# Optimization experiments

Hardware: AMD Instinct MI355X
Metric: run time of the kernel (lower is better)

## Reference

```python
import jax, jax.numpy as jnp
import numpy as np

N_NODES = 100000
N_EDGES = 3200000
F_IN = 128
F_HID = 32
F_OUT = 40


def gcn_conv(x, edge_index, edge_weight, W, b):
    # GCNConv with normalize=False: linear transform, then edge-weighted
    # gather from source nodes and scatter-add into destination nodes.
    h = x @ W                                   # [N, F_out]
    src, dst = edge_index[0], edge_index[1]
    msgs = h[src] * edge_weight[:, None]        # [E, F_out] gather + scale
    agg = jax.ops.segment_sum(msgs, dst, num_segments=N_NODES)
    return agg + b


def setup_inputs() -> dict:
    key = jax.random.key(0)
    k1, k2, k3, k4, k5, k6, k7 = jax.random.split(key, 7)
    x = jax.random.normal(k1, (N_NODES, F_IN), dtype=jnp.float32)
    edge_index = jax.random.randint(k2, (2, N_EDGES), 0, N_NODES, dtype=jnp.int64)
    edge_weight = jax.random.uniform(k3, (N_EDGES,), dtype=jnp.float32)
    # Glorot-style init for layer weights, zeros for biases (PyG defaults)
    W1 = jax.random.normal(k4, (F_IN, F_HID), dtype=jnp.float32) * (1.0 / np.sqrt(F_IN))
    b1 = jnp.zeros((F_HID,), dtype=jnp.float32)
    W2 = jax.random.normal(k5, (F_HID, F_OUT), dtype=jnp.float32) * (1.0 / np.sqrt(F_HID))
    b2 = jnp.zeros((F_OUT,), dtype=jnp.float32)
    return {"x": x, "edge_index": edge_index, "edge_weight": edge_weight,
            "W1": W1, "b1": b1, "W2": W2, "b2": b2}


def reference(x, edge_index, edge_weight, W1, b1, W2, b2):
    h = gcn_conv(x, edge_index, edge_weight, W1, b1)
    h = jax.nn.relu(h)
    # F.dropout(training=self.training) is identity in eval mode
    h = gcn_conv(h, edge_index, edge_weight, W2, b2)
    return jax.nn.log_softmax(h, axis=1)
```

## Files before the change

### kernel.cpp

```cpp
#include <hip/hip_runtime.h>
#include <hip/hip_fp16.h>
#include <math.h>

#define N_NODES 100000
#define N_EDGES 3200000
#define F_IN    128
#define F_HID   32
#define F_OUT   40
#define NBINS   ((N_NODES + 255) >> 8)
#define EPB     4096
#define NBLK    ((N_EDGES + EPB - 1) / EPB)
#define BKT_CAP (N_EDGES + 8 * N_NODES)

typedef _Float16 h2_t __attribute__((ext_vector_type(2)));
__device__ __forceinline__ float fdot2u(unsigned a, unsigned b, float c) {
    return __builtin_amdgcn_fdot2(__builtin_bit_cast(h2_t, a),
                                  __builtin_bit_cast(h2_t, b), c, false);
}

__global__ __launch_bounds__(256) void gemm1_kernel(const float* __restrict__ x,
                                                    const float* __restrict__ W,
                                                    __half* __restrict__ h1h) {
    __shared__ float Ws[F_IN * F_HID];
    __shared__ float Xs[32][F_IN + 4];
    const int tid  = threadIdx.x;
    const int row0 = blockIdx.x * 32;

    for (int i = tid; i < (F_IN * F_HID) / 4; i += 256)
        ((float4*)Ws)[i] = ((const float4*)W)[i];

    for (int i = tid; i < 1024; i += 256) {
        int r = i >> 5;
        int c = i & 31;
        ((float4*)&Xs[r][0])[c] = ((const float4*)x)[(size_t)(row0 + r) * (F_IN / 4) + c];
    }
    __syncthreads();

    const int r  = tid >> 3;
    const int c0 = (tid & 7) * 4;
    float a0 = 0.f, a1 = 0.f, a2 = 0.f, a3 = 0.f;
    for (int k = 0; k < F_IN; ++k) {
        const float xv = Xs[r][k];
        const float* wrow = &Ws[k * F_HID + c0];
        a0 += xv * wrow[0];
        a1 += xv * wrow[1];
        a2 += xv * wrow[2];
        a3 += xv * wrow[3];
    }
    const int row = row0 + r;
    __half2* o = (__half2*)(h1h + (size_t)row * F_HID + c0);
    o[0] = __floats2half2_rn(a0, a1);
    o[1] = __floats2half2_rn(a2, a3);
}

__global__ __launch_bounds__(256) void histA_kernel(const int* __restrict__ ei,
                                                    int* __restrict__ gcnt) {
    __shared__ int lh[NBINS];
    const int tid = threadIdx.x;
    const int e0  = blockIdx.x * EPB;
    for (int i = tid; i < NBINS; i += 256) lh[i] = 0;
    __syncthreads();

    for (int base = 0; base < EPB; base += 1024) {
        const int e = e0 + base + 4 * tid;
        if (e + 3 < N_EDGES) {
            const int4 dv = *(const int4*)&ei[N_EDGES + e];
            atomicAdd(&lh[dv.x >> 8], 1);
            atomicAdd(&lh[dv.y >> 8], 1);
            atomicAdd(&lh[dv.z >> 8], 1);
            atomicAdd(&lh[dv.w >> 8], 1);
        } else {
            for (int k = 0; k < 4; ++k)
                if (e + k < N_EDGES) atomicAdd(&lh[ei[N_EDGES + e + k] >> 8], 1);
        }
    }
    __syncthreads();
    for (int b = tid; b < NBINS; b += 256)
        gcnt[(size_t)blockIdx.x * NBINS + b] = lh[b];
}

__global__ __launch_bounds__(256) void colscan_kernel(const int* __restrict__ gcnt,
                                                      int* __restrict__ pbase,
                                                      int* __restrict__ bintot) {
    __shared__ int s[256];
    __shared__ int carry;
    const int b   = blockIdx.x;
    const int tid = threadIdx.x;
    if (tid == 0) carry = 0;
    __syncthreads();
    for (int c = 0; c < NBLK; c += 256) {
        const int blk = c + tid;
        const int v = (blk < NBLK) ? gcnt[(size_t)blk * NBINS + b] : 0;
        s[tid] = v;
        __syncthreads();
        for (int off = 1; off < 256; off <<= 1) {
            int u = (tid >= off) ? s[tid - off] : 0;
            __syncthreads();
            s[tid] += u;
            __syncthreads();
        }
        if (blk < NBLK) pbase[(size_t)blk * NBINS + b] = carry + s[tid] - v;
        __syncthreads();
        if (tid == 255) carry += s[255];
        __syncthreads();
    }
    if (tid == 0) bintot[b] = carry;
}

__global__ __launch_bounds__(512) void binscan_kernel(const int* __restrict__ bintot,
                                                      int* __restrict__ binbase) {
    __shared__ int s[512];
    const int t = threadIdx.x;
    const int v = (t < NBINS) ? bintot[t] : 0;
    s[t] = v;
    __syncthreads();
    for (int off = 1; off < 512; off <<= 1) {
        int u = (t >= off) ? s[t - off] : 0;
        __syncthreads();
        s[t] += u;
        __syncthreads();
    }
    if (t <= NBINS) binbase[t] = s[t] - v;
}

__global__ __launch_bounds__(256) void placeA_kernel(const int* __restrict__ ei,
                                                     const float* __restrict__ ew,
                                                     const int* __restrict__ gcnt,
                                                     const int* __restrict__ binbase,
                                                     const int* __restrict__ pbase,
                                                     int* __restrict__ stg4,
                                                     unsigned char* __restrict__ dlowg) {
    __shared__ int lhist[512];
    __shared__ int lscan[512];
    __shared__ int lcur[512];
    __shared__ int lwbase[512];
    __shared__ int stmp[256];
    __shared__ int lstg4[EPB];
    __shared__ unsigned short lbin[EPB];
    __shared__ unsigned char ldlow[EPB];
    const int tid = threadIdx.x;
    const int blk = blockIdx.x;
    const int e0  = blk * EPB;
    const int tot = min(EPB, N_EDGES - e0);

    lhist[tid] = 0; lhist[tid + 256] = 0;
    lwbase[tid] = 0; lwbase[tid + 256] = 0;
    __syncthreads();
    for (int b = tid; b < NBINS; b += 256) {
        lhist[b]  = gcnt[(size_t)blk * NBINS + b];
        lwbase[b] = binbase[b] + pbase[(size_t)blk * NBINS + b];
    }
    __syncthreads();

    const int ca = lhist[2 * tid];
    const int cb = lhist[2 * tid + 1];
    const int pair = ca + cb;
    stmp[tid] = pair;
    __syncthreads();
    for (int off = 1; off < 256; off <<= 1) {
        int u = (tid >= off) ? stmp[tid - off] : 0;
        __syncthreads();
        stmp[tid] += u;
        __syncthreads();
    }
    const int pexcl = stmp[tid] - pair;
    lscan[2 * tid]     = pexcl;
    lscan[2 * tid + 1] = pexcl + ca;
    lcur[2 * tid]      = pexcl;
    lcur[2 * tid + 1]  = pexcl + ca;
    __syncthreads();

#define PLACE1(S, D, WF)                                                        \
    {                                                                           \
        const int b = (D) >> 8;                                                 \
        const int p = atomicAdd(&lcur[b], 1);                                   \
        lstg4[p] = (S) | ((int)__half_as_ushort(__float2half(WF)) << 17);       \
        lbin[p] = (unsigned short)b;                                            \
        ldlow[p] = (unsigned char)((D) & 255);                                  \
    }
    for (int base = 0; base < EPB; base += 1024) {
        const int e = e0 + base + 4 * tid;
        if (e + 3 < N_EDGES) {
            const int4   sv = *(const int4*)&ei[e];
            const int4   dv = *(const int4*)&ei[N_EDGES + e];
            const float4 wv = *(const float4*)&ew[e];
            PLACE1(sv.x, dv.x, wv.x);
            PLACE1(sv.y, dv.y, wv.y);
            PLACE1(sv.z, dv.z, wv.z);
            PLACE1(sv.w, dv.w, wv.w);
        } else {
            for (int k = 0; k < 4; ++k)
                if (e + k < N_EDGES)
                    PLACE1(ei[e + k], ei[N_EDGES + e + k], ew[e + k]);
        }
    }
#undef PLACE1
    __syncthreads();

    for (int i = tid; i < tot; i += 256) {
        const int b = lbin[i];
        const int pos = lwbase[b] + (i - lscan[b]);
        stg4[pos] = lstg4[i];
        dlowg[pos] = ldlow[i];
    }
}

__global__ __launch_bounds__(256) void partB1_kernel(const int* __restrict__ binbase,
                                                     const unsigned char* __restrict__ dlowg,
                                                     int* __restrict__ offsIB,
                                                     int* __restrict__ pbt) {
    __shared__ int lcnt[256];
    __shared__ int lsc[256];
    const int tid   = threadIdx.x;
    const int b     = blockIdx.x;
    const int start = binbase[b];
    const int end   = binbase[b + 1];

    lcnt[tid] = 0;
    __syncthreads();
    for (int j = start + tid; j < end; j += 256)
        atomicAdd(&lcnt[dlowg[j]], 1);
    __syncthreads();

    const int padded = (lcnt[tid] + 7) & ~7;
    lsc[tid] = padded;
    __syncthreads();
    for (int off = 1; off < 256; off <<= 1) {
        int u = (tid >= off) ? lsc[tid - off] : 0;
        __syncthreads();
        lsc[tid] += u;
        __syncthreads();
    }
    offsIB[(b << 8) + tid] = lsc[tid] - padded;
    if (tid == 255) pbt[b] = lsc[255];
}

__global__ __launch_bounds__(512) void padscan_kernel(const int* __restrict__ pbt,
                                                      int* __restrict__ pbb,
                                                      int* __restrict__ offs) {
    __shared__ int s[512];
    const int t = threadIdx.x;
    const int v = (t < NBINS) ? pbt[t] : 0;
    s[t] = v;
    __syncthreads();
    for (int off = 1; off < 512; off <<= 1) {
        int u = (t >= off) ? s[t - off] : 0;
        __syncthreads();
        s[t] += u;
        __syncthreads();
    }
    const int excl = s[t] - v;
    if (t <= NBINS) pbb[t] = excl;
    if (t == NBINS) offs[N_NODES] = excl;
}

__global__ __launch_bounds__(256) void partB2_kernel(const int* __restrict__ binbase,
                                                     const int* __restrict__ stg4,
                                                     const unsigned char* __restrict__ dlowg,
                                                     const int* __restrict__ pbb,
                                                     const int* __restrict__ offsIB,
                                                     int* __restrict__ offs,
                                                     int* __restrict__ bkt) {
    __shared__ int lcur[256];
    const int tid  = threadIdx.x;
    const int b    = blockIdx.x;
    const int node = (b << 8) + tid;
    const int base = pbb[b] + offsIB[node];
    const int pend = (tid < 255) ? (pbb[b] + offsIB[node + 1]) : pbb[b + 1];
    lcur[tid] = base;
    if (node < N_NODES) offs[node] = base;
    __syncthreads();

    const int start = binbase[b];
    const int end   = binbase[b + 1];
    for (int j = start + tid; j < end; j += 256) {
        const int word = stg4[j];
        const int pos = atomicAdd(&lcur[dlowg[j]], 1);
        bkt[pos] = word;
    }
    __syncthreads();

    for (int k = lcur[tid]; k < pend; ++k) bkt[k] = 0;
}

__device__ __forceinline__ void gather_grp(const int* __restrict__ bkt,
                                           int j, const int jend,
                                           const char* __restrict__ tbl,
                                           const unsigned sub8,
                                           float& a0, float& a1, float& a2, float& a3) {
#define PAIR_BODY(PX, PY, RA, RB)                                               \
    {                                                                           \
        const unsigned wp = __builtin_amdgcn_perm((unsigned)(PY) >> 17,         \
                                                  (unsigned)(PX) >> 17,         \
                                                  0x05040100u);                 \
        a0 = fdot2u(__builtin_amdgcn_perm((RB).x, (RA).x, 0x05040100u), wp, a0);\
        a1 = fdot2u(__builtin_amdgcn_perm((RB).x, (RA).x, 0x07060302u), wp, a1);\
        a2 = fdot2u(__builtin_amdgcn_perm((RB).y, (RA).y, 0x05040100u), wp, a2);\
        a3 = fdot2u(__builtin_amdgcn_perm((RB).y, (RA).y, 0x07060302u), wp, a3);\
    }
#define TBL(P) (*(const uint2*)(tbl + (((unsigned)(P) & 0x1FFFFu) << 6) + sub8))
    for (; j < jend; j += 8) {
        const int4 p0 = *(const int4*)&bkt[j];
        const int4 p1 = *(const int4*)&bkt[j + 4];
        const uint2 r0 = TBL(p0.x);
        const uint2 r1 = TBL(p0.y);
        const uint2 r2 = TBL(p0.z);
        const uint2 r3 = TBL(p0.w);
        const uint2 r4 = TBL(p1.x);
        const uint2 r5 = TBL(p1.y);
        const uint2 r6 = TBL(p1.z);
        const uint2 r7 = TBL(p1.w);
        PAIR_BODY(p0.x, p0.y, r0, r1);
        PAIR_BODY(p0.z, p0.w, r2, r3);
        PAIR_BODY(p1.x, p1.y, r4, r5);
        PAIR_BODY(p1.z, p1.w, r6, r7);
    }
#undef TBL
#undef PAIR_BODY
}

__global__ __launch_bounds__(256) void gather1_kernel(const int* __restrict__ offs,
                                                      const int* __restrict__ bkt,
                                                      const __half* __restrict__ h1h,
                                                      const float* __restrict__ b1,
                                                      __half* __restrict__ rh) {
    const int tid  = threadIdx.x;
    const int node = blockIdx.x * 32 + (tid >> 3);
    const int sub  = tid & 7;
    const unsigned sub8 = sub * 8;

    float a0 = 0.f, a1 = 0.f, a2 = 0.f, a3 = 0.f;
    gather_grp(bkt, offs[node], offs[node + 1], (const char*)h1h, sub8,
               a0, a1, a2, a3);

    const float4 bb = ((const float4*)b1)[sub];
    a0 = fmaxf(a0 + bb.x, 0.f);
    a1 = fmaxf(a1 + bb.y, 0.f);
    a2 = fmaxf(a2 + bb.z, 0.f);
    a3 = fmaxf(a3 + bb.w, 0.f);
    uint2 o;
    *(__half2*)&o.x = __floats2half2_rn(a0, a1);
    *(__half2*)&o.y = __floats2half2_rn(a2, a3);
    *(uint2*)((char*)rh + (size_t)node * 64 + sub8) = o;
}

__global__ __launch_bounds__(256) void gather2_lsm_kernel(const int* __restrict__ offs,
                                                          const int* __restrict__ bkt,
                                                          const __half* __restrict__ rh,
                                                          const float* __restrict__ W2,
                                                          const float* __restrict__ b2,
                                                          float* __restrict__ out) {
    __shared__ float W2s[F_HID * F_OUT];
    __shared__ float sblk[32][F_HID + 1];
    const int tid = threadIdx.x;
    for (int i = tid; i < F_HID * F_OUT; i += 256) W2s[i] = W2[i];
    __syncthreads();

    const int nn   = tid >> 3;
    const int node = blockIdx.x * 32 + nn;
    const int sub  = tid & 7;
    const unsigned sub8 = sub * 8;

    float a0 = 0.f, a1 = 0.f, a2 = 0.f, a3 = 0.f;
    gather_grp(bkt, offs[node], offs[node + 1], (const char*)rh, sub8,
               a0, a1, a2, a3);

    sblk[nn][sub * 4 + 0] = a0;
    sblk[nn][sub * 4 + 1] = a1;
    sblk[nn][sub * 4 + 2] = a2;
    sblk[nn][sub * 4 + 3] = a3;

    float o0 = b2[sub], o1 = b2[sub + 8], o2 = b2[sub + 16],
          o3 = b2[sub + 24], o4 = b2[sub + 32];
    #pragma unroll
    for (int k = 0; k < F_HID; ++k) {
        const float sv = sblk[nn][k];
        const float* wr = &W2s[k * F_OUT + sub];
        o0 += sv * wr[0];
        o1 += sv * wr[8];
        o2 += sv * wr[16];
        o3 += sv * wr[24];
        o4 += sv * wr[32];
    }

    float m = fmaxf(fmaxf(fmaxf(o0, o1), fmaxf(o2, o3)), o4);
    m = fmaxf(m, __shfl_xor(m, 1));
    m = fmaxf(m, __shfl_xor(m, 2));
    m = fmaxf(m, __shfl_xor(m, 4));
    float ex = __expf(o0 - m) + __expf(o1 - m) + __expf(o2 - m)
             + __expf(o3 - m) + __expf(o4 - m);
    ex += __shfl_xor(ex, 1);
    ex += __shfl_xor(ex, 2);
    ex += __shfl_xor(ex, 4);
    const float ls = m + __logf(ex);

    float* op = out + (size_t)node * F_OUT + sub;
    op[0]  = o0 - ls;
    op[8]  = o1 - ls;
    op[16] = o2 - ls;
    op[24] = o3 - ls;
    op[32] = o4 - ls;
}

extern "C" void kernel_launch(void* const* d_in, const int* in_sizes, int n_in,
                              void* d_out, int out_size, void* d_ws, size_t ws_size,
                              hipStream_t stream) {
    const float* x  = (const float*)d_in[0];
    const int*   ei = (const int*)d_in[1];
    const float* ew = (const float*)d_in[2];
    const float* W1 = (const float*)d_in[3];
    const float* b1 = (const float*)d_in[4];
    const float* W2 = (const float*)d_in[5];
    const float* b2 = (const float*)d_in[6];
    float* out = (float*)d_out;

    char* p = (char*)d_ws;
    size_t off = 0;
    auto alloc = [&](size_t bytes) {
        char* r = p + off;
        off += (bytes + 15) & ~(size_t)15;
        return r;
    };
    int*   gcnt    = (int*)  alloc((size_t)NBLK * NBINS * 4);
    int*   pbase   = (int*)  alloc((size_t)NBLK * NBINS * 4);
    int*   bintot  = (int*)  alloc((size_t)NBINS * 4);
    int*   binbase = (int*)  alloc((size_t)(NBINS + 1) * 4);
    int*   pbt     = (int*)  alloc((size_t)NBINS * 4);
    int*   pbb     = (int*)  alloc((size_t)(NBINS + 1) * 4);
    int*   offsIB  = (int*)  alloc((size_t)NBINS * 256 * 4);
    int*   offs    = (int*)  alloc((size_t)(N_NODES + 1) * 4);
    int*   bkt     = (int*)  alloc((size_t)BKT_CAP * 4);
    char*  uni     = (char*) alloc((size_t)N_EDGES * 5);
    int*   stg4    = (int*)uni;
    unsigned char* dlowg = (unsigned char*)(uni + (size_t)N_EDGES * 4);
    __half* h1h    = (__half*)uni;
    __half* rh     = h1h + (size_t)N_NODES * F_HID;

    histA_kernel<<<NBLK, 256, 0, stream>>>(ei, gcnt);
    colscan_kernel<<<NBINS, 256, 0, stream>>>(gcnt, pbase, bintot);
    binscan_kernel<<<1, 512, 0, stream>>>(bintot, binbase);
    placeA_kernel<<<NBLK, 256, 0, stream>>>(ei, ew, gcnt, binbase, pbase, stg4, dlowg);
    partB1_kernel<<<NBINS, 256, 0, stream>>>(binbase, dlowg, offsIB, pbt);
    padscan_kernel<<<1, 512, 0, stream>>>(pbt, pbb, offs);
    partB2_kernel<<<NBINS, 256, 0, stream>>>(binbase, stg4, dlowg, pbb, offsIB, offs, bkt);

    gemm1_kernel<<<N_NODES / 32, 256, 0, stream>>>(x, W1, h1h);
    gather1_kernel<<<N_NODES / 32, 256, 0, stream>>>(offs, bkt, h1h, b1, rh);

    gather2_lsm_kernel<<<N_NODES / 32, 256, 0, stream>>>(offs, bkt, rh, W2, b2, out);
}
```

Before: 197.9 us.

## Split CSR buckets by source-node half to improve gather locality

Each node's destination bucket is split into two sub-lists: edges whose source is below 50000 and edges whose source is at or above it. Each gather kernel first walks the low-source list, then the high-source list. The goal is a smaller working set of gathered feature rows in each phase, so more hits land in L2/MALL. In exchange there is extra metadata (a 16-bit tag per edge), two prefix scans, duplicated offset arrays, and more per-node padding, which adds padded work items and loop overhead in the gathers.

```diff
diff --git a/kernel.cpp b/kernel.cpp
--- a/kernel.cpp
+++ b/kernel.cpp
@@ -10,7 +10,8 @@
 #define NBINS   ((N_NODES + 255) >> 8)
 #define EPB     4096
 #define NBLK    ((N_EDGES + EPB - 1) / EPB)
-#define BKT_CAP (N_EDGES + 8 * N_NODES)
+#define SRC_SPLIT 50000
+#define CAPH    (N_EDGES / 2 + 8 * N_NODES)
 
 typedef _Float16 h2_t __attribute__((ext_vector_type(2)));
 __device__ __forceinline__ float fdot2u(unsigned a, unsigned b, float c) {
@@ -129,7 +130,7 @@
                                                      const int* __restrict__ binbase,
                                                      const int* __restrict__ pbase,
                                                      int* __restrict__ stg4,
-                                                     unsigned char* __restrict__ dlowg) {
+                                                     unsigned short* __restrict__ metag) {
     __shared__ int lhist[512];
     __shared__ int lscan[512];
     __shared__ int lcur[512];
@@ -137,7 +138,7 @@
     __shared__ int stmp[256];
     __shared__ int lstg4[EPB];
     __shared__ unsigned short lbin[EPB];
-    __shared__ unsigned char ldlow[EPB];
+    __shared__ unsigned short lmeta[EPB];
     const int tid = threadIdx.x;
     const int blk = blockIdx.x;
     const int e0  = blk * EPB;
@@ -176,7 +177,7 @@
         const int p = atomicAdd(&lcur[b], 1);                                   \
         lstg4[p] = (S) | ((int)__half_as_ushort(__float2half(WF)) << 17);       \
         lbin[p] = (unsigned short)b;                                            \
-        ldlow[p] = (unsigned char)((D) & 255);                                  \
+        lmeta[p] = (unsigned short)(((D) & 255) | (((S) >= SRC_SPLIT) << 8));   \
     }
     for (int base = 0; base < EPB; base += 1024) {
         const int e = e0 + base + 4 * tid;
@@ -201,29 +202,33 @@
         const int b = lbin[i];
         const int pos = lwbase[b] + (i - lscan[b]);
         stg4[pos] = lstg4[i];
-        dlowg[pos] = ldlow[i];
+        metag[pos] = lmeta[i];
     }
 }
 
 __global__ __launch_bounds__(256) void partB1_kernel(const int* __restrict__ binbase,
-                                                     const unsigned char* __restrict__ dlowg,
-                                                     int* __restrict__ offsIB,
-                                                     int* __restrict__ pbt) {
-    __shared__ int lcnt[256];
-    __shared__ int lsc[256];
+                                                     const unsigned short* __restrict__ metag,
+                                                     int* __restrict__ offsIBA,
+                                                     int* __restrict__ offsIBB,
+                                                     int* __restrict__ pbtA,
+                                                     int* __restrict__ pbtB) {
+    __shared__ int lcA[256], lcB[256], lsc[256];
     const int tid   = threadIdx.x;
     const int b     = blockIdx.x;
     const int start = binbase[b];
     const int end   = binbase[b + 1];
 
-    lcnt[tid] = 0;
-    __syncthreads();
-    for (int j = start + tid; j < end; j += 256)
-        atomicAdd(&lcnt[dlowg[j]], 1);
-    __syncthreads();
-
-    const int padded = (lcnt[tid] + 7) & ~7;
-    lsc[tid] = padded;
+    lcA[tid] = 0; lcB[tid] = 0;
+    __syncthreads();
+    for (int j = start + tid; j < end; j += 256) {
+        const unsigned m = metag[j];
+        if (m & 256) atomicAdd(&lcB[m & 255], 1);
+        else         atomicAdd(&lcA[m & 255], 1);
+    }
+    __syncthreads();
+
+    const int padA = (lcA[tid] + 7) & ~7;
+    lsc[tid] = padA;
     __syncthreads();
     for (int off = 1; off < 256; off <<= 1) {
         int u = (tid >= off) ? lsc[tid - off] : 0;
@@ -231,56 +236,101 @@
         lsc[tid] += u;
         __syncthreads();
     }
-    offsIB[(b << 8) + tid] = lsc[tid] - padded;
-    if (tid == 255) pbt[b] = lsc[255];
-}
-
-__global__ __launch_bounds__(512) void padscan_kernel(const int* __restrict__ pbt,
-                                                      int* __restrict__ pbb,
-                                                      int* __restrict__ offs) {
+    offsIBA[(b << 8) + tid] = lsc[tid] - padA;
+    if (tid == 255) pbtA[b] = lsc[255];
+    __syncthreads();
+
+    const int padB = (lcB[tid] + 7) & ~7;
+    lsc[tid] = padB;
+    __syncthreads();
+    for (int off = 1; off < 256; off <<= 1) {
+        int u = (tid >= off) ? lsc[tid - off] : 0;
+        __syncthreads();
+        lsc[tid] += u;
+        __syncthreads();
+    }
+    offsIBB[(b << 8) + tid] = lsc[tid] - padB;
+    if (tid == 255) pbtB[b] = lsc[255];
+}
+
+__global__ __launch_bounds__(512) void padscan2_kernel(const int* __restrict__ pbtA,
+                                                       const int* __restrict__ pbtB,
+                                                       int* __restrict__ pbbA,
+                                                       int* __restrict__ pbbB,
+                                                       int* __restrict__ offsA,
+                                                       int* __restrict__ offsB) {
     __shared__ int s[512];
     const int t = threadIdx.x;
-    const int v = (t < NBINS) ? pbt[t] : 0;
-    s[t] = v;
-    __syncthreads();
-    for (int off = 1; off < 512; off <<= 1) {
-        int u = (t >= off) ? s[t - off] : 0;
-        __syncthreads();
-        s[t] += u;
-        __syncthreads();
-    }
-    const int excl = s[t] - v;
-    if (t <= NBINS) pbb[t] = excl;
-    if (t == NBINS) offs[N_NODES] = excl;
+    {
+        const int v = (t < NBINS) ? pbtA[t] : 0;
+        s[t] = v;
+        __syncthreads();
+        for (int off = 1; off < 512; off <<= 1) {
+            int u = (t >= off) ? s[t - off] : 0;
+            __syncthreads();
+            s[t] += u;
+            __syncthreads();
+        }
+        if (t <= NBINS) pbbA[t] = s[t] - v;
+        if (t == NBINS) offsA[N_NODES] = s[t] - v;
+        __syncthreads();
+    }
+    {
+        const int v = (t < NBINS) ? pbtB[t] : 0;
+        s[t] = v;
+        __syncthreads();
+        for (int off = 1; off < 512; off <<= 1) {
+            int u = (t >= off) ? s[t - off] : 0;
+            __syncthreads();
+            s[t] += u;
+            __syncthreads();
+        }
+        if (t <= NBINS) pbbB[t] = s[t] - v;
+        if (t == NBINS) offsB[N_NODES] = s[t] - v;
+    }
 }
 
 __global__ __launch_bounds__(256) void partB2_kernel(const int* __restrict__ binbase,
                                                      const int* __restrict__ stg4,
-                                                     const unsigned char* __restrict__ dlowg,
-                                                     const int* __restrict__ pbb,
-                                                     const int* __restrict__ offsIB,
-                                                     int* __restrict__ offs,
-                                                     int* __restrict__ bkt) {
-    __shared__ int lcur[256];
+                                                     const unsigned short* __restrict__ metag,
+                                                     const int* __restrict__ pbbA,
+                                                     const int* __restrict__ pbbB,
+                                                     const int* __restrict__ offsIBA,
+                                                     const int* __restrict__ offsIBB,
+                                                     int* __restrict__ offsA,
+                                                     int* __restrict__ offsB,
+                                                     int* __restrict__ bktA,
+                                                     int* __restrict__ bktB) {
+    __shared__ int lcurA[256], lcurB[256];
     const int tid  = threadIdx.x;
     const int b    = blockIdx.x;
     const int node = (b << 8) + tid;
-    const int base = pbb[b] + offsIB[node];
-    const int pend = (tid < 255) ? (pbb[b] + offsIB[node + 1]) : pbb[b + 1];
-    lcur[tid] = base;
-    if (node < N_NODES) offs[node] = base;
+    const int baseA = pbbA[b] + offsIBA[node];
+    const int baseB = pbbB[b] + offsIBB[node];
+    const int pendA = (tid < 255) ? (pbbA[b] + offsIBA[node + 1]) : pbbA[b + 1];
+    const int pendB = (tid < 255) ? (pbbB[b] + offsIBB[node + 1]) : pbbB[b + 1];
+    lcurA[tid] = baseA;
+    lcurB[tid] = baseB;
+    if (node < N_NODES) { offsA[node] = baseA; offsB[node] = baseB; }
     __syncthreads();
 
     const int start = binbase[b];
     const int end   = binbase[b + 1];
     for (int j = start + tid; j < end; j += 256) {
         const int word = stg4[j];
-        const int pos = atomicAdd(&lcur[dlowg[j]], 1);
-        bkt[pos] = word;
-    }
-    __syncthreads();
-
-    for (int k = lcur[tid]; k < pend; ++k) bkt[k] = 0;
+        const unsigned m = metag[j];
+        if (m & 256) {
+            const int pos = atomicAdd(&lcurB[m & 255], 1);
+            bktB[pos] = word;
+        } else {
+            const int pos = atomicAdd(&lcurA[m & 255], 1);
+            bktA[pos] = word;
+        }
+    }
+    __syncthreads();
+
+    for (int k = lcurA[tid]; k < pendA; ++k) bktA[k] = 0;
+    for (int k = lcurB[tid]; k < pendB; ++k) bktB[k] = SRC_SPLIT;
 }
 
 __device__ __forceinline__ void gather_grp(const int* __restrict__ bkt,
@@ -319,8 +369,10 @@
 #undef PAIR_BODY
 }
 
-__global__ __launch_bounds__(256) void gather1_kernel(const int* __restrict__ offs,
-                                                      const int* __restrict__ bkt,
+__global__ __launch_bounds__(256) void gather1_kernel(const int* __restrict__ offsA,
+                                                      const int* __restrict__ offsB,
+                                                      const int* __restrict__ bktA,
+                                                      const int* __restrict__ bktB,
                                                       const __half* __restrict__ h1h,
                                                       const float* __restrict__ b1,
                                                       __half* __restrict__ rh) {
@@ -330,7 +382,9 @@
     const unsigned sub8 = sub * 8;
 
     float a0 = 0.f, a1 = 0.f, a2 = 0.f, a3 = 0.f;
-    gather_grp(bkt, offs[node], offs[node + 1], (const char*)h1h, sub8,
+    gather_grp(bktA, offsA[node], offsA[node + 1], (const char*)h1h, sub8,
+               a0, a1, a2, a3);
+    gather_grp(bktB, offsB[node], offsB[node + 1], (const char*)h1h, sub8,
                a0, a1, a2, a3);
 
     const float4 bb = ((const float4*)b1)[sub];
@@ -344,8 +398,10 @@
     *(uint2*)((char*)rh + (size_t)node * 64 + sub8) = o;
 }
 
-__global__ __launch_bounds__(256) void gather2_lsm_kernel(const int* __restrict__ offs,
-                                                          const int* __restrict__ bkt,
+__global__ __launch_bounds__(256) void gather2_lsm_kernel(const int* __restrict__ offsA,
+                                                          const int* __restrict__ offsB,
+                                                          const int* __restrict__ bktA,
+                                                          const int* __restrict__ bktB,
                                                           const __half* __restrict__ rh,
                                                           const float* __restrict__ W2,
                                                           const float* __restrict__ b2,
@@ -362,7 +418,9 @@
     const unsigned sub8 = sub * 8;
 
     float a0 = 0.f, a1 = 0.f, a2 = 0.f, a3 = 0.f;
-    gather_grp(bkt, offs[node], offs[node + 1], (const char*)rh, sub8,
+    gather_grp(bktA, offsA[node], offsA[node + 1], (const char*)rh, sub8,
+               a0, a1, a2, a3);
+    gather_grp(bktB, offsB[node], offsB[node + 1], (const char*)rh, sub8,
                a0, a1, a2, a3);
 
     sblk[nn][sub * 4 + 0] = a0;
@@ -425,27 +483,33 @@
     int*   pbase   = (int*)  alloc((size_t)NBLK * NBINS * 4);
     int*   bintot  = (int*)  alloc((size_t)NBINS * 4);
     int*   binbase = (int*)  alloc((size_t)(NBINS + 1) * 4);
-    int*   pbt     = (int*)  alloc((size_t)NBINS * 4);
-    int*   pbb     = (int*)  alloc((size_t)(NBINS + 1) * 4);
-    int*   offsIB  = (int*)  alloc((size_t)NBINS * 256 * 4);
-    int*   offs    = (int*)  alloc((size_t)(N_NODES + 1) * 4);
-    int*   bkt     = (int*)  alloc((size_t)BKT_CAP * 4);
-    char*  uni     = (char*) alloc((size_t)N_EDGES * 5);
+    int*   pbtA    = (int*)  alloc((size_t)NBINS * 4);
+    int*   pbtB    = (int*)  alloc((size_t)NBINS * 4);
+    int*   pbbA    = (int*)  alloc((size_t)(NBINS + 1) * 4);
+    int*   pbbB    = (int*)  alloc((size_t)(NBINS + 1) * 4);
+    int*   offsIBA = (int*)  alloc((size_t)NBINS * 256 * 4);
+    int*   offsIBB = (int*)  alloc((size_t)NBINS * 256 * 4);
+    int*   offsA   = (int*)  alloc((size_t)(N_NODES + 1) * 4);
+    int*   offsB   = (int*)  alloc((size_t)(N_NODES + 1) * 4);
+    int*   bktA    = (int*)  alloc((size_t)CAPH * 4);
+    int*   bktB    = (int*)  alloc((size_t)CAPH * 4);
+    char*  uni     = (char*) alloc((size_t)N_EDGES * 6);
     int*   stg4    = (int*)uni;
-    unsigned char* dlowg = (unsigned char*)(uni + (size_t)N_EDGES * 4);
+    unsigned short* metag = (unsigned short*)(uni + (size_t)N_EDGES * 4);
     __half* h1h    = (__half*)uni;
     __half* rh     = h1h + (size_t)N_NODES * F_HID;
 
     histA_kernel<<<NBLK, 256, 0, stream>>>(ei, gcnt);
     colscan_kernel<<<NBINS, 256, 0, stream>>>(gcnt, pbase, bintot);
     binscan_kernel<<<1, 512, 0, stream>>>(bintot, binbase);
-    placeA_kernel<<<NBLK, 256, 0, stream>>>(ei, ew, gcnt, binbase, pbase, stg4, dlowg);
-    partB1_kernel<<<NBINS, 256, 0, stream>>>(binbase, dlowg, offsIB, pbt);
-    padscan_kernel<<<1, 512, 0, stream>>>(pbt, pbb, offs);
-    partB2_kernel<<<NBINS, 256, 0, stream>>>(binbase, stg4, dlowg, pbb, offsIB, offs, bkt);
+    placeA_kernel<<<NBLK, 256, 0, stream>>>(ei, ew, gcnt, binbase, pbase, stg4, metag);
+    partB1_kernel<<<NBINS, 256, 0, stream>>>(binbase, metag, offsIBA, offsIBB, pbtA, pbtB);
+    padscan2_kernel<<<1, 512, 0, stream>>>(pbtA, pbtB, pbbA, pbbB, offsA, offsB);
+    partB2_kernel<<<NBINS, 256, 0, stream>>>(binbase, stg4, metag, pbbA, pbbB,
+                                             offsIBA, offsIBB, offsA, offsB, bktA, bktB);
 
     gemm1_kernel<<<N_NODES / 32, 256, 0, stream>>>(x, W1, h1h);
-    gather1_kernel<<<N_NODES / 32, 256, 0, stream>>>(offs, bkt, h1h, b1, rh);
-
-    gather2_lsm_kernel<<<N_NODES / 32, 256, 0, stream>>>(offs, bkt, rh, W2, b2, out);
-}
+    gather1_kernel<<<N_NODES / 32, 256, 0, stream>>>(offsA, offsB, bktA, bktB, h1h, b1, rh);
+
+    gather2_lsm_kernel<<<N_NODES / 32, 256, 0, stream>>>(offsA, offsB, bktA, bktB, rh, W2, b2, out);
+}
```

After: 177.5 us. 10.3% less time.
